# Kernel tuning notes

Hardware: AMD Instinct MI355X
Metric: run time of the kernel (lower is better)

## Reference

```python
import jax, jax.numpy as jnp
import numpy as np

N, D, E, L, H, F1, G, A = 4096, 256, 131072, 3, 4, 128, 16, 32

def setup_inputs() -> dict:
    key = jax.random.key(0)
    ks = jax.random.split(key, 12)
    s = lambda k, shape, fan: jax.random.normal(k, shape, jnp.float32) / np.sqrt(fan)
    return {
        "x": jax.random.normal(ks[0], (N, D), jnp.float32),
        "edge_attr": jax.random.uniform(ks[1], (E,), jnp.float32),
        "conv_Wself": s(ks[2], (L, D, D), D),
        "conv_Wnbr": s(ks[3], (L, D, D), D),
        "conv_b": jnp.zeros((L, D), jnp.float32),
        "bn_gamma": jnp.ones((L - 1, D), jnp.float32),
        "bn_beta": jnp.zeros((L - 1, D), jnp.float32),
        "bn_mean": jnp.zeros((L - 1, D), jnp.float32),
        "bn_var": jnp.ones((L - 1, D), jnp.float32),
        "Wqkv": s(ks[4], (3, D, D), D),
        "bqkv": jnp.zeros((3, D), jnp.float32),
        "Wo": s(ks[5], (D, D), D),
        "bo": jnp.zeros((D,), jnp.float32),
        "fc1_W": s(ks[6], (D, F1), D),
        "fc1_b": jnp.zeros((F1,), jnp.float32),
        "AW1": s(ks[7], (G, F1, A), F1),
        "Ab1": jnp.zeros((G, A), jnp.float32),
        "AW2": s(ks[8], (G, A, 1), A),
        "Ab2": jnp.zeros((G, 1), jnp.float32),
        "edge_index": jax.random.randint(ks[9], (2, E), 0, N, jnp.int32),
        "node_groups": jax.random.randint(ks[10], (N,), 0, G, jnp.int32),
    }


def reference(x, edge_attr, conv_Wself, conv_Wnbr, conv_b, bn_gamma, bn_beta,
              bn_mean, bn_var, Wqkv, bqkv, Wo, bo, fc1_W, fc1_b,
              AW1, Ab1, AW2, Ab2, edge_index, node_groups):
    src, dst = edge_index[0], edge_index[1]
    # message-passing conv stack (edge_attr only used by the last, non-attention layer)
    for i in range(L):
        msg = x[src]
        if i == L - 1:
            msg = msg * edge_attr[:, None]
        agg = jax.ops.segment_sum(msg, dst, num_segments=N)
        x = x @ conv_Wself[i] + agg @ conv_Wnbr[i] + conv_b[i]
        if i < L - 1:
            x = bn_gamma[i] * (x - bn_mean[i]) * jax.lax.rsqrt(bn_var[i] + 1e-5) + bn_beta[i]
            x = jax.nn.elu(x)
    # hierarchy self-attention over all N nodes (batch of 1), residual add
    dh = D // H
    q = (x @ Wqkv[0] + bqkv[0]).reshape(N, H, dh)
    k = (x @ Wqkv[1] + bqkv[1]).reshape(N, H, dh)
    v = (x @ Wqkv[2] + bqkv[2]).reshape(N, H, dh)
    scores = jnp.einsum('nhd,mhd->hnm', q, k) / np.sqrt(dh).astype(np.float32)
    attn = jax.nn.softmax(scores, axis=-1)
    o = jnp.einsum('hnm,mhd->nhd', attn, v).reshape(N, D) @ Wo + bo
    x = x + o
    feats = jax.nn.elu(x @ fc1_W + fc1_b)  # [N, F1]; dropout is eval no-op
    # MoE-style per-node group adapter routing: gather tiny MLP weights per node
    h = jax.nn.relu(jnp.einsum('nd,nda->na', feats, AW1[node_groups]) + Ab1[node_groups])
    out = jnp.einsum('na,nao->no', h, AW2[node_groups]) + Ab2[node_groups]  # [N, 1]
    return out
```

## Files before the change

### kernel.cpp

```cpp
#include <hip/hip_runtime.h>
#include <math.h>

#define NN   4096
#define DIM  256
#define NE   131072
#define NH   4
#define DH   64
#define F1D  128
#define NG   16
#define AD   32

typedef unsigned short u16;
typedef unsigned int   u32;
typedef _Float16 f16;
typedef __attribute__((ext_vector_type(8))) _Float16 half8;
typedef __attribute__((ext_vector_type(4))) float f32x4;

enum { EPI_BIAS = 0, EPI_BNELU = 1 };
enum { MEPI_WO = 0, MEPI_FC1 = 1 };

#define MFMA16(a, b, c) __builtin_amdgcn_mfma_f32_16x16x32_f16(a, b, c, 0, 0, 0)

__device__ inline u16 f2h(float x) { union { f16 f; u16 u; } c; c.f = (f16)x; return c.u; }
__device__ inline void split16(float x, u16& h, u16& l) {
    union { f16 f; u16 u; } ch, cl;
    ch.f = (f16)x;
    cl.f = (f16)(x - (float)ch.f);
    h = ch.u; l = cl.u;
}

__global__ void csr_count(const int* __restrict__ dst, int* __restrict__ cnt) {
    int e = blockIdx.x * 256 + threadIdx.x;
    atomicAdd(&cnt[dst[e]], 1);
}

__global__ __launch_bounds__(1024) void csr_scan(
    int* __restrict__ cnt, int* __restrict__ off)
{
    __shared__ int wsum[16];
    const int t = threadIdx.x;
    const int lane = t & 63;
    int4 v = *(const int4*)&cnt[t * 4];
    const int s = v.x + v.y + v.z + v.w;
    int acc = s;
    #pragma unroll
    for (int o = 1; o < 64; o <<= 1) {
        int u = __shfl_up(acc, o);
        if (lane >= o) acc += u;
    }
    if (lane == 63) wsum[t >> 6] = acc;
    __syncthreads();
    if (t < 16) {
        int w0 = wsum[t];
        int a2 = w0;
        #pragma unroll
        for (int o = 1; o < 16; o <<= 1) {
            int u = __shfl_up(a2, o);
            if (t >= o) a2 += u;
        }
        wsum[t] = a2 - w0;
    }
    __syncthreads();
    const int base = wsum[t >> 6] + (acc - s);
    off[t * 4 + 0] = base;
    off[t * 4 + 1] = base + v.x;
    off[t * 4 + 2] = base + v.x + v.y;
    off[t * 4 + 3] = base + v.x + v.y + v.z;
    *(int4*)&cnt[t * 4] = make_int4(0, 0, 0, 0);
    if (t == 1023) off[NN] = base + s;
}

__global__ void csr_fill(const int* __restrict__ dst, const int* __restrict__ src,
                         const float* __restrict__ eattr, const int* __restrict__ off,
                         int* __restrict__ cur, int* __restrict__ esrc,
                         float* __restrict__ ewt) {
    int e = blockIdx.x * 256 + threadIdx.x;
    int d = dst[e];
    int pos = off[d] + atomicAdd(&cur[d], 1);
    esrc[pos] = src[e];
    ewt[pos]  = eattr[e];
}

__global__ __launch_bounds__(256) void prep_kernel(
    const float* __restrict__ x,
    const float* __restrict__ Ws, const float* __restrict__ Wn,
    const float* __restrict__ Wqkv, const float* __restrict__ Wo,
    const float* __restrict__ fc1W,
    u16* __restrict__ xh, u16* __restrict__ xl,
    u16* __restrict__ wch, u16* __restrict__ wcl,
    u16* __restrict__ w4h, u16* __restrict__ w4l,
    u16* __restrict__ f1h, u16* __restrict__ f1l,
    int* __restrict__ cur)
{
    const int b = blockIdx.x;
    const int t = threadIdx.x;
    if (b < 1024) {
        const int gid = b * 256 + t;
        const float4 v = *(const float4*)&x[(size_t)gid * 4];
        u16 h[4], l[4];
        split16(v.x, h[0], l[0]); split16(v.y, h[1], l[1]);
        split16(v.z, h[2], l[2]); split16(v.w, h[3], l[3]);
        *(uint2*)&xh[(size_t)gid * 4] =
            make_uint2((u32)h[0] | ((u32)h[1] << 16), (u32)h[2] | ((u32)h[3] << 16));
        *(uint2*)&xl[(size_t)gid * 4] =
            make_uint2((u32)l[0] | ((u32)l[1] << 16), (u32)l[2] | ((u32)l[3] << 16));
    } else if (b < 1408) {
        const int gid = (b - 1024) * 256 + t;
        const int L = gid / 32768;
        const int rem = gid % 32768;
        const int m = rem / 128;
        const int k4 = (rem % 128) * 4;
        const float* S = Ws + (size_t)L * 65536;
        const float* Nb = Wn + (size_t)L * 65536;
        u16 h[4], l[4];
        #pragma unroll
        for (int j = 0; j < 4; ++j) {
            const int k = k4 + j;
            const float v = (k < 256) ? S[(size_t)k * 256 + m]
                                      : Nb[(size_t)(k - 256) * 256 + m];
            split16(v, h[j], l[j]);
        }
        const size_t o = (size_t)L * 131072 + (size_t)m * 512 + k4;
        *(uint2*)&wch[o] = make_uint2((u32)h[0] | ((u32)h[1] << 16), (u32)h[2] | ((u32)h[3] << 16));
        *(uint2*)&wcl[o] = make_uint2((u32)l[0] | ((u32)l[1] << 16), (u32)l[2] | ((u32)l[3] << 16));
    } else if (b < 1664) {
        const int gid = (b - 1408) * 256 + t;
        const int mat = gid / 16384;
        const int rem = gid % 16384;
        const int m = rem / 64;
        const int k4 = (rem % 64) * 4;
        const float* W = (mat < 3) ? Wqkv + (size_t)mat * 65536 : Wo;
        u16 h[4], l[4];
        #pragma unroll
        for (int j = 0; j < 4; ++j)
            split16(W[(size_t)(k4 + j) * 256 + m], h[j], l[j]);
        const size_t o = (size_t)mat * 65536 + (size_t)m * 256 + k4;
        *(uint2*)&w4h[o] = make_uint2((u32)h[0] | ((u32)h[1] << 16), (u32)h[2] | ((u32)h[3] << 16));
        *(uint2*)&w4l[o] = make_uint2((u32)l[0] | ((u32)l[1] << 16), (u32)l[2] | ((u32)l[3] << 16));
    } else if (b < 1696) {
        const int gid = (b - 1664) * 256 + t;
        const int m = gid / 64;
        const int k4 = (gid % 64) * 4;
        u16 h[4], l[4];
        #pragma unroll
        for (int j = 0; j < 4; ++j)
            split16(fc1W[(size_t)(k4 + j) * F1D + m], h[j], l[j]);
        const size_t o = (size_t)m * 256 + k4;
        *(uint2*)&f1h[o] = make_uint2((u32)h[0] | ((u32)h[1] << 16), (u32)h[2] | ((u32)h[3] << 16));
        *(uint2*)&f1l[o] = make_uint2((u32)l[0] | ((u32)l[1] << 16), (u32)l[2] | ((u32)l[3] << 16));
    } else {
        const int gid = (b - 1696) * 256 + t;
        if (gid < NN / 4) *(int4*)&cur[gid * 4] = make_int4(0, 0, 0, 0);
    }
}

template<bool LAST>
__global__ __launch_bounds__(256) void agg_kernel(
    const float* __restrict__ x, const int* __restrict__ esrc,
    const float* __restrict__ ewt, const int* __restrict__ off,
    u16* __restrict__ aggh, u16* __restrict__ aggl)
{
    const int node = blockIdx.x * 4 + (threadIdx.x >> 6);
    const int lane = threadIdx.x & 63;
    const int d4 = lane * 4;
    int j = off[node];
    const int j1 = off[node + 1];
    float4 acc = make_float4(0.f, 0.f, 0.f, 0.f);
    for (; j + 4 <= j1; j += 4) {
        const int s0 = esrc[j], s1 = esrc[j + 1], s2 = esrc[j + 2], s3 = esrc[j + 3];
        const float4 x0 = *(const float4*)&x[(size_t)s0 * DIM + d4];
        const float4 x1 = *(const float4*)&x[(size_t)s1 * DIM + d4];
        const float4 x2 = *(const float4*)&x[(size_t)s2 * DIM + d4];
        const float4 x3 = *(const float4*)&x[(size_t)s3 * DIM + d4];
        const float w0 = LAST ? ewt[j]     : 1.f;
        const float w1 = LAST ? ewt[j + 1] : 1.f;
        const float w2 = LAST ? ewt[j + 2] : 1.f;
        const float w3 = LAST ? ewt[j + 3] : 1.f;
        acc.x = fmaf(x0.x, w0, acc.x); acc.y = fmaf(x0.y, w0, acc.y);
        acc.z = fmaf(x0.z, w0, acc.z); acc.w = fmaf(x0.w, w0, acc.w);
        acc.x = fmaf(x1.x, w1, acc.x); acc.y = fmaf(x1.y, w1, acc.y);
        acc.z = fmaf(x1.z, w1, acc.z); acc.w = fmaf(x1.w, w1, acc.w);
        acc.x = fmaf(x2.x, w2, acc.x); acc.y = fmaf(x2.y, w2, acc.y);
        acc.z = fmaf(x2.z, w2, acc.z); acc.w = fmaf(x2.w, w2, acc.w);
        acc.x = fmaf(x3.x, w3, acc.x); acc.y = fmaf(x3.y, w3, acc.y);
        acc.z = fmaf(x3.z, w3, acc.z); acc.w = fmaf(x3.w, w3, acc.w);
    }
    for (; j < j1; ++j) {
        const int s = esrc[j];
        const float w = LAST ? ewt[j] : 1.f;
        const float4 xv = *(const float4*)&x[(size_t)s * DIM + d4];
        acc.x = fmaf(xv.x, w, acc.x); acc.y = fmaf(xv.y, w, acc.y);
        acc.z = fmaf(xv.z, w, acc.z); acc.w = fmaf(xv.w, w, acc.w);
    }
    u16 h[4], l[4];
    split16(acc.x, h[0], l[0]); split16(acc.y, h[1], l[1]);
    split16(acc.z, h[2], l[2]); split16(acc.w, h[3], l[3]);
    *(uint2*)&aggh[(size_t)node * DIM + d4] =
        make_uint2((u32)h[0] | ((u32)h[1] << 16), (u32)h[2] | ((u32)h[3] << 16));
    *(uint2*)&aggl[(size_t)node * DIM + d4] =
        make_uint2((u32)l[0] | ((u32)l[1] << 16), (u32)l[2] | ((u32)l[3] << 16));
}

template<int EPI>
__global__ __launch_bounds__(256) void conv_mfma(
    const u16* __restrict__ xh, const u16* __restrict__ xl,
    const u16* __restrict__ gh, const u16* __restrict__ gl,
    const u16* __restrict__ bth, const u16* __restrict__ btl,
    const float* __restrict__ bias,
    const float* __restrict__ gamma, const float* __restrict__ beta,
    const float* __restrict__ bnmean, const float* __restrict__ bnvar,
    float* __restrict__ outf, u16* __restrict__ oh, u16* __restrict__ ol)
{
    __shared__ u16 lds[4 * 4608];
    u16* As_h = lds;
    u16* As_l = lds + 4608;
    u16* Bs_h = lds + 9216;
    u16* Bs_l = lds + 13824;
    #define TKP 72

    const int tid  = threadIdx.x;
    const int row0 = blockIdx.y * 64;
    const int col0 = blockIdx.x * 64;

    const int w   = tid >> 6;
    const int l15 = tid & 15, h4 = (tid & 63) >> 4;
    const int rh  = w & 1, ch = w >> 1;
    const int lrow = tid & 63, lseg = tid >> 6;
    const int lc = lseg * 16;

    uint4 sah0, sah1, sal0, sal1, sbh0, sbh1, sbl0, sbl1;
    {
        const u16* pah = xh + (size_t)(row0 + lrow) * DIM + lc;
        const u16* pal = xl + (size_t)(row0 + lrow) * DIM + lc;
        const u16* pbh = bth + (size_t)(col0 + lrow) * 512 + lc;
        const u16* pbl = btl + (size_t)(col0 + lrow) * 512 + lc;
        sah0 = ((const uint4*)pah)[0]; sah1 = ((const uint4*)pah)[1];
        sal0 = ((const uint4*)pal)[0]; sal1 = ((const uint4*)pal)[1];
        sbh0 = ((const uint4*)pbh)[0]; sbh1 = ((const uint4*)pbh)[1];
        sbl0 = ((const uint4*)pbl)[0]; sbl1 = ((const uint4*)pbl)[1];
    }

    const f32x4 z4 = {0.f, 0.f, 0.f, 0.f};
    f32x4 acc[2][2] = {{z4, z4}, {z4, z4}};

    for (int kt = 0; kt < 8; ++kt) {
        *(uint4*)&As_h[lrow * TKP + lc]     = sah0;
        *(uint4*)&As_h[lrow * TKP + lc + 8] = sah1;
        *(uint4*)&As_l[lrow * TKP + lc]     = sal0;
        *(uint4*)&As_l[lrow * TKP + lc + 8] = sal1;
        *(uint4*)&Bs_h[lrow * TKP + lc]     = sbh0;
        *(uint4*)&Bs_h[lrow * TKP + lc + 8] = sbh1;
        *(uint4*)&Bs_l[lrow * TKP + lc]     = sbl0;
        *(uint4*)&Bs_l[lrow * TKP + lc + 8] = sbl1;
        if (kt + 1 < 8) {
            const int kn = kt + 1;
            const u16 *pah, *pal;
            if (kn < 4) {
                pah = xh + (size_t)(row0 + lrow) * DIM + kn * 64 + lc;
                pal = xl + (size_t)(row0 + lrow) * DIM + kn * 64 + lc;
            } else {
                pah = gh + (size_t)(row0 + lrow) * DIM + (kn - 4) * 64 + lc;
                pal = gl + (size_t)(row0 + lrow) * DIM + (kn - 4) * 64 + lc;
            }
            const u16* pbh = bth + (size_t)(col0 + lrow) * 512 + kn * 64 + lc;
            const u16* pbl = btl + (size_t)(col0 + lrow) * 512 + kn * 64 + lc;
            sah0 = ((const uint4*)pah)[0]; sah1 = ((const uint4*)pah)[1];
            sal0 = ((const uint4*)pal)[0]; sal1 = ((const uint4*)pal)[1];
            sbh0 = ((const uint4*)pbh)[0]; sbh1 = ((const uint4*)pbh)[1];
            sbl0 = ((const uint4*)pbl)[0]; sbl1 = ((const uint4*)pbl)[1];
        }
        __syncthreads();

        __builtin_amdgcn_s_setprio(1);
        #pragma unroll
        for (int kc = 0; kc < 2; ++kc) {
            const int dc = kc * 32 + h4 * 8;
            half8 afh[2], afl[2], bfh[2], bfl[2];
            #pragma unroll
            for (int ab = 0; ab < 2; ++ab) {
                const int r = rh * 32 + ab * 16 + l15;
                afh[ab] = *(const half8*)&As_h[r * TKP + dc];
                afl[ab] = *(const half8*)&As_l[r * TKP + dc];
            }
            #pragma unroll
            for (int bb = 0; bb < 2; ++bb) {
                const int r = ch * 32 + bb * 16 + l15;
                bfh[bb] = *(const half8*)&Bs_h[r * TKP + dc];
                bfl[bb] = *(const half8*)&Bs_l[r * TKP + dc];
            }
            #pragma unroll
            for (int ab = 0; ab < 2; ++ab)
                #pragma unroll
                for (int bb = 0; bb < 2; ++bb) {
                    acc[ab][bb] = MFMA16(afh[ab], bfh[bb], acc[ab][bb]);
                    acc[ab][bb] = MFMA16(afh[ab], bfl[bb], acc[ab][bb]);
                    acc[ab][bb] = MFMA16(afl[ab], bfh[bb], acc[ab][bb]);
                }
        }
        __builtin_amdgcn_s_setprio(0);
        __syncthreads();
    }

    #pragma unroll
    for (int ab = 0; ab < 2; ++ab)
        #pragma unroll
        for (int bb = 0; bb < 2; ++bb) {
            const int c  = col0 + ch * 32 + bb * 16 + l15;
            const int r0 = row0 + rh * 32 + ab * 16 + h4 * 4;
            #pragma unroll
            for (int i = 0; i < 4; ++i) {
                const int r = r0 + i;
                float t = acc[ab][bb][i] + bias[c];
                if (EPI == EPI_BNELU) {
                    t = gamma[c] * (t - bnmean[c]) * rsqrtf(bnvar[c] + 1e-5f) + beta[c];
                    t = t > 0.f ? t : expm1f(t);
                }
                outf[(size_t)r * DIM + c] = t;
                u16 hh, ll;
                split16(t, hh, ll);
                oh[(size_t)r * DIM + c] = hh;
                ol[(size_t)r * DIM + c] = ll;
            }
        }
    #undef TKP
}

__global__ __launch_bounds__(256) void qkv_mfma(
    const u16* __restrict__ xh, const u16* __restrict__ xl,
    const u16* __restrict__ wth, const u16* __restrict__ wtl,
    const float* __restrict__ bias,
    u16* __restrict__ qh_o, u16* __restrict__ ql_o,
    u16* __restrict__ kh_o, u16* __restrict__ kl_o,
    u16* __restrict__ vt_o)
{
    __shared__ u16 lds[4 * 4608];
    u16* As_h = lds;
    u16* As_l = lds + 4608;
    u16* Bs_h = lds + 9216;
    u16* Bs_l = lds + 13824;
    #define TKP 72

    const int tid  = threadIdx.x;
    const int row0 = blockIdx.y * 64;
    const int mat  = blockIdx.x >> 2;
    const int col0 = (blockIdx.x & 3) * 64;
    const float* biasp = bias + mat * DIM;

    const int w   = tid >> 6;
    const int l15 = tid & 15, h4 = (tid & 63) >> 4;
    const int rh  = w & 1, ch = w >> 1;
    const int lrow = tid & 63, lseg = tid >> 6;
    const int lc = lseg * 16;

    const size_t brow = (size_t)(mat * 256 + col0 + lrow) * 256;
    uint4 sah0, sah1, sal0, sal1, sbh0, sbh1, sbl0, sbl1;
    {
        const u16* pah = xh + (size_t)(row0 + lrow) * DIM + lc;
        const u16* pal = xl + (size_t)(row0 + lrow) * DIM + lc;
        sah0 = ((const uint4*)pah)[0]; sah1 = ((const uint4*)pah)[1];
        sal0 = ((const uint4*)pal)[0]; sal1 = ((const uint4*)pal)[1];
        sbh0 = ((const uint4*)(wth + brow + lc))[0]; sbh1 = ((const uint4*)(wth + brow + lc))[1];
        sbl0 = ((const uint4*)(wtl + brow + lc))[0]; sbl1 = ((const uint4*)(wtl + brow + lc))[1];
    }

    const f32x4 z4 = {0.f, 0.f, 0.f, 0.f};
    f32x4 acc[2][2] = {{z4, z4}, {z4, z4}};

    for (int kt = 0; kt < 4; ++kt) {
        *(uint4*)&As_h[lrow * TKP + lc]     = sah0;
        *(uint4*)&As_h[lrow * TKP + lc + 8] = sah1;
        *(uint4*)&As_l[lrow * TKP + lc]     = sal0;
        *(uint4*)&As_l[lrow * TKP + lc + 8] = sal1;
        *(uint4*)&Bs_h[lrow * TKP + lc]     = sbh0;
        *(uint4*)&Bs_h[lrow * TKP + lc + 8] = sbh1;
        *(uint4*)&Bs_l[lrow * TKP + lc]     = sbl0;
        *(uint4*)&Bs_l[lrow * TKP + lc + 8] = sbl1;
        if (kt + 1 < 4) {
            const int kb = (kt + 1) * 64 + lc;
            const u16* pah = xh + (size_t)(row0 + lrow) * DIM + kb;
            const u16* pal = xl + (size_t)(row0 + lrow) * DIM + kb;
            sah0 = ((const uint4*)pah)[0]; sah1 = ((const uint4*)pah)[1];
            sal0 = ((const uint4*)pal)[0]; sal1 = ((const uint4*)pal)[1];
            sbh0 = ((const uint4*)(wth + brow + kb))[0]; sbh1 = ((const uint4*)(wth + brow + kb))[1];
            sbl0 = ((const uint4*)(wtl + brow + kb))[0]; sbl1 = ((const uint4*)(wtl + brow + kb))[1];
        }
        __syncthreads();

        __builtin_amdgcn_s_setprio(1);
        #pragma unroll
        for (int kc = 0; kc < 2; ++kc) {
            const int dc = kc * 32 + h4 * 8;
            half8 afh[2], afl[2], bfh[2], bfl[2];
            #pragma unroll
            for (int ab = 0; ab < 2; ++ab) {
                const int r = rh * 32 + ab * 16 + l15;
                afh[ab] = *(const half8*)&As_h[r * TKP + dc];
                afl[ab] = *(const half8*)&As_l[r * TKP + dc];
            }
            #pragma unroll
            for (int bb = 0; bb < 2; ++bb) {
                const int r = ch * 32 + bb * 16 + l15;
                bfh[bb] = *(const half8*)&Bs_h[r * TKP + dc];
                bfl[bb] = *(const half8*)&Bs_l[r * TKP + dc];
            }
            #pragma unroll
            for (int ab = 0; ab < 2; ++ab)
                #pragma unroll
                for (int bb = 0; bb < 2; ++bb) {
                    acc[ab][bb] = MFMA16(afh[ab], bfh[bb], acc[ab][bb]);
                    acc[ab][bb] = MFMA16(afh[ab], bfl[bb], acc[ab][bb]);
                    acc[ab][bb] = MFMA16(afl[ab], bfh[bb], acc[ab][bb]);
                }
        }
        __builtin_amdgcn_s_setprio(0);
        __syncthreads();
    }

    const float s = (mat == 0) ? 0.125f : 1.0f;
    u16* oph = (mat == 0) ? qh_o : kh_o;
    u16* opl = (mat == 0) ? ql_o : kl_o;
    #pragma unroll
    for (int ab = 0; ab < 2; ++ab)
        #pragma unroll
        for (int bb = 0; bb < 2; ++bb) {
            const int c  = col0 + ch * 32 + bb * 16 + l15;
            const int r0 = row0 + rh * 32 + ab * 16 + h4 * 4;
            if (mat < 2) {
                #pragma unroll
                for (int i = 0; i < 4; ++i) {
                    const int r = r0 + i;
                    const float t = (acc[ab][bb][i] + biasp[c]) * s;
                    u16 hh, ll;
                    split16(t, hh, ll);
                    oph[(size_t)r * DIM + c] = hh;
                    opl[(size_t)r * DIM + c] = ll;
                }
            } else {
                u16 v[4];
                #pragma unroll
                for (int i = 0; i < 4; ++i)
                    v[i] = f2h(acc[ab][bb][i] + biasp[c]);
                *(uint2*)&vt_o[(size_t)c * NN + r0] =
                    make_uint2((u32)v[0] | ((u32)v[1] << 16), (u32)v[2] | ((u32)v[3] << 16));
            }
        }
    #undef TKP
}

template<int MEPI>
__global__ __launch_bounds__(256) void mfma_gemm(
    const u16* __restrict__ Ah, const u16* __restrict__ Al,
    const u16* __restrict__ Bth, const u16* __restrict__ Btl,
    const float* __restrict__ bias, const float* __restrict__ resid,
    float* __restrict__ outf, u16* __restrict__ outh, u16* __restrict__ outl,
    int K, int M)
{
    __shared__ u16 lds[4 * 4608];
    u16* As_h = lds;
    u16* As_l = lds + 4608;
    u16* Bs_h = lds + 9216;
    u16* Bs_l = lds + 13824;
    #define TKP 72

    const int tid  = threadIdx.x;
    const int row0 = blockIdx.y * 64;
    const int col0 = blockIdx.x * 64;

    const int w   = tid >> 6;
    const int l15 = tid & 15, h4 = (tid & 63) >> 4;
    const int rh  = w & 1, ch = w >> 1;
    const int lrow = tid & 63, lseg = tid >> 6;
    const int lc = lseg * 16;

    uint4 sah0, sah1, sal0, sal1, sbh0, sbh1, sbl0, sbl1;
    {
        const u16* pa0 = Ah  + (size_t)(row0 + lrow) * K + lc;
        const u16* pa1 = Al  + (size_t)(row0 + lrow) * K + lc;
        const u16* pb0 = Bth + (size_t)(col0 + lrow) * K + lc;
        const u16* pb1 = Btl + (size_t)(col0 + lrow) * K + lc;
        sah0 = ((const uint4*)pa0)[0]; sah1 = ((const uint4*)pa0)[1];
        sal0 = ((const uint4*)pa1)[0]; sal1 = ((const uint4*)pa1)[1];
        sbh0 = ((const uint4*)pb0)[0]; sbh1 = ((const uint4*)pb0)[1];
        sbl0 = ((const uint4*)pb1)[0]; sbl1 = ((const uint4*)pb1)[1];
    }

    const f32x4 z4 = {0.f, 0.f, 0.f, 0.f};
    f32x4 acc[2][2] = {{z4, z4}, {z4, z4}};
    const int NKT2 = K / 64;

    for (int kt = 0; kt < NKT2; ++kt) {
        *(uint4*)&As_h[lrow * TKP + lc]     = sah0;
        *(uint4*)&As_h[lrow * TKP + lc + 8] = sah1;
        *(uint4*)&As_l[lrow * TKP + lc]     = sal0;
        *(uint4*)&As_l[lrow * TKP + lc + 8] = sal1;
        *(uint4*)&Bs_h[lrow * TKP + lc]     = sbh0;
        *(uint4*)&Bs_h[lrow * TKP + lc + 8] = sbh1;
        *(uint4*)&Bs_l[lrow * TKP + lc]     = sbl0;
        *(uint4*)&Bs_l[lrow * TKP + lc + 8] = sbl1;
        if (kt + 1 < NKT2) {
            const int kb = (kt + 1) * 64 + lc;
            const u16* pa0 = Ah  + (size_t)(row0 + lrow) * K + kb;
            const u16* pa1 = Al  + (size_t)(row0 + lrow) * K + kb;
            const u16* pb0 = Bth + (size_t)(col0 + lrow) * K + kb;
            const u16* pb1 = Btl + (size_t)(col0 + lrow) * K + kb;
            sah0 = ((const uint4*)pa0)[0]; sah1 = ((const uint4*)pa0)[1];
            sal0 = ((const uint4*)pa1)[0]; sal1 = ((const uint4*)pa1)[1];
            sbh0 = ((const uint4*)pb0)[0]; sbh1 = ((const uint4*)pb0)[1];
            sbl0 = ((const uint4*)pb1)[0]; sbl1 = ((const uint4*)pb1)[1];
        }
        __syncthreads();

        __builtin_amdgcn_s_setprio(1);
        #pragma unroll
        for (int kc = 0; kc < 2; ++kc) {
            const int dc = kc * 32 + h4 * 8;
            half8 afh[2], afl[2], bfh[2], bfl[2];
            #pragma unroll
            for (int ab = 0; ab < 2; ++ab) {
                const int r = rh * 32 + ab * 16 + l15;
                afh[ab] = *(const half8*)&As_h[r * TKP + dc];
                afl[ab] = *(const half8*)&As_l[r * TKP + dc];
            }
            #pragma unroll
            for (int bb = 0; bb < 2; ++bb) {
                const int r = ch * 32 + bb * 16 + l15;
                bfh[bb] = *(const half8*)&Bs_h[r * TKP + dc];
                bfl[bb] = *(const half8*)&Bs_l[r * TKP + dc];
            }
            #pragma unroll
            for (int ab = 0; ab < 2; ++ab)
                #pragma unroll
                for (int bb = 0; bb < 2; ++bb) {
                    acc[ab][bb] = MFMA16(afh[ab], bfh[bb], acc[ab][bb]);
                    acc[ab][bb] = MFMA16(afh[ab], bfl[bb], acc[ab][bb]);
                    acc[ab][bb] = MFMA16(afl[ab], bfh[bb], acc[ab][bb]);
                }
        }
        __builtin_amdgcn_s_setprio(0);
        __syncthreads();
    }

    #pragma unroll
    for (int ab = 0; ab < 2; ++ab)
        #pragma unroll
        for (int bb = 0; bb < 2; ++bb) {
            const int c  = col0 + ch * 32 + bb * 16 + l15;
            const int r0 = row0 + rh * 32 + ab * 16 + h4 * 4;
            #pragma unroll
            for (int i = 0; i < 4; ++i) {
                const int r = r0 + i;
                float t = acc[ab][bb][i] + bias[c];
                if (MEPI == MEPI_WO) {
                    t += resid[(size_t)r * M + c];
                    u16 hh, ll;
                    split16(t, hh, ll);
                    outh[(size_t)r * M + c] = hh;
                    outl[(size_t)r * M + c] = ll;
                } else {
                    t = t > 0.f ? t : expm1f(t);
                    outf[(size_t)r * M + c] = t;
                }
            }
        }
    #undef TKP
}

#define QB 64
#define KB 64
#define NSPLIT 4
#define NKT (NN / KB)
#define KP 72

__global__ __launch_bounds__(256, 3) void attn_kernel(
    const u16* __restrict__ qhi, const u16* __restrict__ qlo,
    const u16* __restrict__ khi, const u16* __restrict__ klo,
    const u16* __restrict__ vT,
    float* __restrict__ op0, float* __restrict__ op1,
    float* __restrict__ op2, float* __restrict__ op3,
    float* __restrict__ mpart, float* __restrict__ lpart)
{
    __shared__ u16 lds[18560];
    u16* Kh = lds;
    u16* Kl = lds + 4608;
    u16* Vt = lds + 9216;
    u16* Pb = lds + 13824;
    u16* Qh = lds;
    u16* Ql = lds + 4608;
    float* frow = (float*)(lds + 18432);

    const int tid = threadIdx.x;
    const int h   = blockIdx.y;
    const int q0  = blockIdx.x * QB;
    const int sp  = blockIdx.z;
    const int kt0 = sp * (NKT / NSPLIT);
    const int kt1 = kt0 + NKT / NSPLIT;

    const int w   = tid >> 6;
    const int l   = tid & 63;
    const int l15 = l & 15, h4 = l >> 4;

    const int lrow = tid & 63, lseg = tid >> 6;
    const int gq = h * DH + lseg * 16;

    {
        const u16* s0 = qhi + (size_t)(q0 + lrow) * DIM + gq;
        const u16* s1 = qlo + (size_t)(q0 + lrow) * DIM + gq;
        uint4 a = ((const uint4*)s0)[0], b = ((const uint4*)s0)[1];
        uint4 c = ((const uint4*)s1)[0], d = ((const uint4*)s1)[1];
        *(uint4*)&Qh[lrow * KP + lseg * 16]     = a;
        *(uint4*)&Qh[lrow * KP + lseg * 16 + 8] = b;
        *(uint4*)&Ql[lrow * KP + lseg * 16]     = c;
        *(uint4*)&Ql[lrow * KP + lseg * 16 + 8] = d;
    }

    auto load_tile = [&](int kt_ld, uint4& k0, uint4& k1, uint4& l0, uint4& l1,
                         uint4& v0, uint4& v1) {
        const int key0 = kt_ld * KB;
        const u16* s0 = khi + (size_t)(key0 + lrow) * DIM + gq;
        const u16* s1 = klo + (size_t)(key0 + lrow) * DIM + gq;
        const u16* s2 = vT + (size_t)(h * DH + lrow) * NN + key0 + lseg * 16;
        k0 = ((const uint4*)s0)[0]; k1 = ((const uint4*)s0)[1];
        l0 = ((const uint4*)s1)[0]; l1 = ((const uint4*)s1)[1];
        v0 = ((const uint4*)s2)[0]; v1 = ((const uint4*)s2)[1];
    };

    uint4 kA0, kA1, lA0, lA1, vA0, vA1;
    uint4 kB0, kB1, lB0, lB1, vB0, vB1;
    load_tile(kt0,     kA0, kA1, lA0, lA1, vA0, vA1);
    load_tile(kt0 + 1, kB0, kB1, lB0, lB1, vB0, vB1);
    __syncthreads();

    half8 qf[2][2];
    #pragma unroll
    for (int kc = 0; kc < 2; ++kc) {
        const int r = w * 16 + l15;
        const int dc = kc * 32 + h4 * 8;
        qf[kc][0] = *(const half8*)&Qh[r * KP + dc];
        qf[kc][1] = *(const half8*)&Ql[r * KP + dc];
    }
    __syncthreads();

    const f32x4 z4 = {0.f, 0.f, 0.f, 0.f};
    f32x4 oacc[4] = {z4, z4, z4, z4};
    float m_run[4], l_run[4];
    #pragma unroll
    for (int i = 0; i < 4; ++i) { m_run[i] = -3.0e38f; l_run[i] = 0.f; }

    auto tile_body = [&](uint4& k0, uint4& k1, uint4& l0, uint4& l1,
                         uint4& v0, uint4& v1, int ldnext) {
        *(uint4*)&Kh[lrow * KP + lseg * 16]     = k0;
        *(uint4*)&Kh[lrow * KP + lseg * 16 + 8] = k1;
        *(uint4*)&Kl[lrow * KP + lseg * 16]     = l0;
        *(uint4*)&Kl[lrow * KP + lseg * 16 + 8] = l1;
        *(uint4*)&Vt[lrow * KP + lseg * 16]     = v0;
        *(uint4*)&Vt[lrow * KP + lseg * 16 + 8] = v1;
        if (ldnext < kt1)
            load_tile(ldnext, k0, k1, l0, l1, v0, v1);
        __syncthreads();

        f32x4 sc[4] = {z4, z4, z4, z4};
        __builtin_amdgcn_s_setprio(1);
        #pragma unroll
        for (int kc = 0; kc < 2; ++kc) {
            const int dc = kc * 32 + h4 * 8;
            half8 kfh[4], kfl[4];
            #pragma unroll
            for (int kcb = 0; kcb < 4; ++kcb) {
                const int r = kcb * 16 + l15;
                kfh[kcb] = *(const half8*)&Kh[r * KP + dc];
                kfl[kcb] = *(const half8*)&Kl[r * KP + dc];
            }
            #pragma unroll
            for (int kcb = 0; kcb < 4; ++kcb) {
                sc[kcb] = MFMA16(qf[kc][0], kfh[kcb], sc[kcb]);
                sc[kcb] = MFMA16(qf[kc][0], kfl[kcb], sc[kcb]);
                sc[kcb] = MFMA16(qf[kc][1], kfh[kcb], sc[kcb]);
            }
        }
        __builtin_amdgcn_s_setprio(0);
        float p[4][4], fr[4];
        #pragma unroll
        for (int i = 0; i < 4; ++i) {
            float pm = fmaxf(fmaxf(sc[0][i], sc[1][i]), fmaxf(sc[2][i], sc[3][i]));
            #pragma unroll
            for (int off = 1; off < 16; off <<= 1)
                pm = fmaxf(pm, __shfl_xor(pm, off));
            const float mnew = fmaxf(m_run[i], pm);
            fr[i] = __expf(m_run[i] - mnew);
            m_run[i] = mnew;
            p[0][i] = __expf(sc[0][i] - mnew);
            p[1][i] = __expf(sc[1][i] - mnew);
            p[2][i] = __expf(sc[2][i] - mnew);
            p[3][i] = __expf(sc[3][i] - mnew);
            float ls = (p[0][i] + p[1][i]) + (p[2][i] + p[3][i]);
            #pragma unroll
            for (int off = 1; off < 16; off <<= 1) ls += __shfl_xor(ls, off);
            l_run[i] = l_run[i] * fr[i] + ls;
        }
        #pragma unroll
        for (int kcb = 0; kcb < 4; ++kcb) {
            const int kk = kcb * 16 + l15;
            #pragma unroll
            for (int i = 0; i < 4; ++i)
                Pb[(w * 16 + h4 * 4 + i) * KP + kk] = f2h(p[kcb][i]);
        }
        if (l15 == 0) {
            #pragma unroll
            for (int i = 0; i < 4; ++i)
                frow[w * 16 + h4 * 4 + i] = fr[i];
        }
        const float frq = frow[w * 16 + l15];
        #pragma unroll
        for (int db = 0; db < 4; ++db) oacc[db] *= frq;
        __builtin_amdgcn_s_setprio(1);
        #pragma unroll
        for (int kc = 0; kc < 2; ++kc) {
            const half8 pf = *(const half8*)&Pb[(w * 16 + l15) * KP + kc * 32 + h4 * 8];
            #pragma unroll
            for (int db = 0; db < 4; ++db) {
                const half8 vf = *(const half8*)&Vt[(db * 16 + l15) * KP + kc * 32 + h4 * 8];
                oacc[db] = MFMA16(vf, pf, oacc[db]);
            }
        }
        __builtin_amdgcn_s_setprio(0);
        __syncthreads();
    };

    for (int kt = kt0; kt < kt1; kt += 2) {
        tile_body(kA0, kA1, lA0, lA1, vA0, vA1, kt + 2);
        tile_body(kB0, kB1, lB0, lB1, vB0, vB1, kt + 3);
    }

    float* ob = (sp == 0) ? op0 : ((sp == 1) ? op1 : ((sp == 2) ? op2 : op3));
    #pragma unroll
    for (int db = 0; db < 4; ++db)
        *(f32x4*)&ob[(size_t)(q0 + w * 16 + l15) * DIM + h * DH + db * 16 + h4 * 4] = oacc[db];
    if (l15 == 0) {
        #pragma unroll
        for (int i = 0; i < 4; ++i) {
            const int r = w * 16 + h4 * 4 + i;
            mpart[((size_t)sp * NN + q0 + r) * NH + h] = m_run[i];
            lpart[((size_t)sp * NN + q0 + r) * NH + h] = l_run[i];
        }
    }
}

__global__ __launch_bounds__(256) void attn_combine(
    const float* __restrict__ o0, const float* __restrict__ o1,
    const float* __restrict__ o2, const float* __restrict__ o3,
    const float* __restrict__ mp, const float* __restrict__ lp,
    u16* __restrict__ ohi, u16* __restrict__ olo)
{
    const int gid = blockIdx.x * 256 + threadIdx.x;
    const int row = gid >> 6;
    const int c4  = (gid & 63) * 4;
    const int h   = c4 >> 6;
    float m[4], wgt[4];
    #pragma unroll
    for (int z = 0; z < 4; ++z) m[z] = mp[((size_t)z * NN + row) * NH + h];
    const float M = fmaxf(fmaxf(m[0], m[1]), fmaxf(m[2], m[3]));
    float den = 0.f;
    #pragma unroll
    for (int z = 0; z < 4; ++z) {
        wgt[z] = __expf(m[z] - M);
        den += lp[((size_t)z * NN + row) * NH + h] * wgt[z];
    }
    const float inv = 1.f / den;
    const float4 a = *(const float4*)&o0[(size_t)row * DIM + c4];
    const float4 b = *(const float4*)&o1[(size_t)row * DIM + c4];
    const float4 c = *(const float4*)&o2[(size_t)row * DIM + c4];
    const float4 d = *(const float4*)&o3[(size_t)row * DIM + c4];
    float r[4];
    r[0] = (a.x * wgt[0] + b.x * wgt[1] + c.x * wgt[2] + d.x * wgt[3]) * inv;
    r[1] = (a.y * wgt[0] + b.y * wgt[1] + c.y * wgt[2] + d.y * wgt[3]) * inv;
    r[2] = (a.z * wgt[0] + b.z * wgt[1] + c.z * wgt[2] + d.z * wgt[3]) * inv;
    r[3] = (a.w * wgt[0] + b.w * wgt[1] + c.w * wgt[2] + d.w * wgt[3]) * inv;
    u16 hh[4], ll[4];
    #pragma unroll
    for (int j = 0; j < 4; ++j) split16(r[j], hh[j], ll[j]);
    *(uint2*)&ohi[(size_t)row * DIM + c4] =
        make_uint2((u32)hh[0] | ((u32)hh[1] << 16), (u32)hh[2] | ((u32)hh[3] << 16));
    *(uint2*)&olo[(size_t)row * DIM + c4] =
        make_uint2((u32)ll[0] | ((u32)ll[1] << 16), (u32)ll[2] | ((u32)ll[3] << 16));
}

__global__ __launch_bounds__(64) void adapter_kernel(
    const float* __restrict__ feats, const int* __restrict__ grp,
    const float* __restrict__ AW1, const float* __restrict__ Ab1,
    const float* __restrict__ AW2, const float* __restrict__ Ab2,
    float* __restrict__ out)
{
    const int n = blockIdx.x;
    const int lane = threadIdx.x;
    __shared__ float f[F1D];
    f[lane]      = feats[(size_t)n * F1D + lane];
    f[lane + 64] = feats[(size_t)n * F1D + 64 + lane];
    __syncthreads();
    const int g = grp[n];
    const float* W1 = AW1 + (size_t)g * F1D * AD;
    const int a = lane & 31;
    const int half = lane >> 5;
    float hsum = 0.f;
    for (int d = 0; d < 64; ++d)
        hsum = fmaf(f[half * 64 + d], W1[(half * 64 + d) * AD + a], hsum);
    hsum += __shfl_xor(hsum, 32);
    hsum = fmaxf(hsum + Ab1[g * AD + a], 0.f);
    float p = hsum * AW2[g * AD + a];
    #pragma unroll
    for (int mm = 1; mm < 32; mm <<= 1) p += __shfl_xor(p, mm);
    if (lane == 0) out[n] = p + Ab2[g];
}

extern "C" void kernel_launch(void* const* d_in, const int* in_sizes, int n_in,
                              void* d_out, int out_size, void* d_ws, size_t ws_size,
                              hipStream_t stream)
{
    const float* x_in   = (const float*)d_in[0];
    const float* eattr  = (const float*)d_in[1];
    const float* Wself  = (const float*)d_in[2];
    const float* Wnbr   = (const float*)d_in[3];
    const float* convb  = (const float*)d_in[4];
    const float* gamma  = (const float*)d_in[5];
    const float* beta   = (const float*)d_in[6];
    const float* bnmean = (const float*)d_in[7];
    const float* bnvar  = (const float*)d_in[8];
    const float* Wqkv   = (const float*)d_in[9];
    const float* bqkv   = (const float*)d_in[10];
    const float* Wo     = (const float*)d_in[11];
    const float* bo     = (const float*)d_in[12];
    const float* fc1W   = (const float*)d_in[13];
    const float* fc1b   = (const float*)d_in[14];
    const float* AW1    = (const float*)d_in[15];
    const float* Ab1    = (const float*)d_in[16];
    const float* AW2    = (const float*)d_in[17];
    const float* Ab2    = (const float*)d_in[18];
    const int*   eidx   = (const int*)d_in[19];
    const int*   grp    = (const int*)d_in[20];
    const int* srcArr = eidx;
    const int* dstArr = eidx + NE;

    float* fws = (float*)d_ws;
    const size_t NM = (size_t)NN * DIM;
    float* bufA  = fws;
    float* bufB  = fws + NM;
    float* bufC  = fws + 2 * NM;
    float* feats = fws + 3 * NM;
    float* mpart = fws + 3 * NM + NM / 2;
    float* lpart = mpart + 4 * NN * NH;
    u16* up = (u16*)(lpart + 4 * NN * NH);
    u16* xpAh = up;             u16* xpAl = xpAh + NM;
    u16* xpBh = xpAl + NM;      u16* xpBl = xpBh + NM;
    u16* aggh = xpBl + NM;      u16* aggl = aggh + NM;
    u16* qh = aggl + NM;        u16* ql = qh + NM;
    u16* kh = ql + NM;          u16* kl = kh + NM;
    u16* vt = kl + NM;
    u16* wcath = vt + NM;
    u16* wcatl = wcath + 3 * 131072;
    u16* wt4h  = wcatl + 3 * 131072;
    u16* wt4l  = wt4h + 4 * 65536;
    u16* fc1h  = wt4l + 4 * 65536;
    u16* fc1l  = fc1h + 32768;
    int*   esrc = (int*)(fc1l + 32768);
    float* ewt  = (float*)(esrc + NE);
    int* off    = (int*)(ewt + NE);
    int* cur    = off + NN + 1;
    float* outp = (float*)d_out;

    float* op2 = (float*)xpAh;
    float* op3 = (float*)xpBh;

    prep_kernel<<<1700, 256, 0, stream>>>(
        x_in, Wself, Wnbr, Wqkv, Wo, fc1W,
        xpAh, xpAl, wcath, wcatl, wt4h, wt4l, fc1h, fc1l, cur);

    csr_count<<<NE / 256, 256, 0, stream>>>(dstArr, cur);
    csr_scan<<<1, 1024, 0, stream>>>(cur, off);
    csr_fill<<<NE / 256, 256, 0, stream>>>(dstArr, srcArr, eattr, off, cur, esrc, ewt);

    const dim3 gc(DIM / 64, NN / 64);
    const int rgrid = NN * DIM / 4 / 256;

    agg_kernel<false><<<NN / 4, 256, 0, stream>>>(x_in, esrc, ewt, off, aggh, aggl);
    conv_mfma<EPI_BNELU><<<gc, 256, 0, stream>>>(
        xpAh, xpAl, aggh, aggl, wcath, wcatl, convb,
        gamma, beta, bnmean, bnvar, bufA, xpBh, xpBl);
    agg_kernel<false><<<NN / 4, 256, 0, stream>>>(bufA, esrc, ewt, off, aggh, aggl);
    conv_mfma<EPI_BNELU><<<gc, 256, 0, stream>>>(
        xpBh, xpBl, aggh, aggl, wcath + 131072, wcatl + 131072, convb + DIM,
        gamma + DIM, beta + DIM, bnmean + DIM, bnvar + DIM, bufC, xpAh, xpAl);
    agg_kernel<true><<<NN / 4, 256, 0, stream>>>(bufC, esrc, ewt, off, aggh, aggl);
    conv_mfma<EPI_BIAS><<<gc, 256, 0, stream>>>(
        xpAh, xpAl, aggh, aggl, wcath + 262144, wcatl + 262144, convb + 2 * DIM,
        nullptr, nullptr, nullptr, nullptr, bufA, xpBh, xpBl);

    qkv_mfma<<<dim3(12, NN / 64), 256, 0, stream>>>(
        xpBh, xpBl, wt4h, wt4l, bqkv, qh, ql, kh, kl, vt);

    attn_kernel<<<dim3(NN / QB, NH, NSPLIT), 256, 0, stream>>>(
        qh, ql, kh, kl, vt, bufB, bufC, op2, op3, mpart, lpart);
    attn_combine<<<rgrid, 256, 0, stream>>>(
        bufB, bufC, op2, op3, mpart, lpart, qh, ql);

    mfma_gemm<MEPI_WO><<<gc, 256, 0, stream>>>(
        qh, ql, wt4h + 3 * 65536, wt4l + 3 * 65536, bo, bufA,
        nullptr, kh, kl, DIM, DIM);

    mfma_gemm<MEPI_FC1><<<dim3(F1D / 64, NN / 64), 256, 0, stream>>>(
        kh, kl, fc1h, fc1l, fc1b, nullptr, feats, nullptr, nullptr, DIM, F1D);

    adapter_kernel<<<NN, 64, 0, stream>>>(feats, grp, AW1, Ab1, AW2, Ab2, outp);
}
```

Before: 244.5 us.

## Double-buffer K/V tiles in attention LDS and halve conv GEMM row tile

The attention kernel now keeps two LDS buffers for the K/V tiles. It stages the next tile into the alternate buffer while computing on the current one, which drops the register-held second tile and the barrier between staging and compute. Occupancy is lowered to 2 blocks per SM to make room for the larger LDS. Separately, the conv GEMM row tile shrinks from 64 to 32 rows, doubling the grid to improve CU utilisation on this small problem, at the cost of more B-tile reloads.

```diff
diff --git a/kernel.cpp b/kernel.cpp
--- a/kernel.cpp
+++ b/kernel.cpp
@@ -211,61 +211,58 @@
     const float* __restrict__ bnmean, const float* __restrict__ bnvar,
     float* __restrict__ outf, u16* __restrict__ oh, u16* __restrict__ ol)
 {
-    __shared__ u16 lds[4 * 4608];
+    __shared__ u16 lds[13824];
     u16* As_h = lds;
-    u16* As_l = lds + 4608;
-    u16* Bs_h = lds + 9216;
-    u16* Bs_l = lds + 13824;
+    u16* As_l = lds + 2304;
+    u16* Bs_h = lds + 4608;
+    u16* Bs_l = lds + 9216;
     #define TKP 72
 
     const int tid  = threadIdx.x;
-    const int row0 = blockIdx.y * 64;
+    const int row0 = blockIdx.y * 32;
     const int col0 = blockIdx.x * 64;
 
     const int w   = tid >> 6;
     const int l15 = tid & 15, h4 = (tid & 63) >> 4;
     const int rh  = w & 1, ch = w >> 1;
-    const int lrow = tid & 63, lseg = tid >> 6;
-    const int lc = lseg * 16;
-
-    uint4 sah0, sah1, sal0, sal1, sbh0, sbh1, sbl0, sbl1;
+    const int arow = tid >> 3, acs = (tid & 7) * 8;
+    const int brow = tid & 63, bseg = tid >> 6;
+    const int bc = bseg * 16;
+
+    uint4 sah, sal, sbh0, sbh1, sbl0, sbl1;
     {
-        const u16* pah = xh + (size_t)(row0 + lrow) * DIM + lc;
-        const u16* pal = xl + (size_t)(row0 + lrow) * DIM + lc;
-        const u16* pbh = bth + (size_t)(col0 + lrow) * 512 + lc;
-        const u16* pbl = btl + (size_t)(col0 + lrow) * 512 + lc;
-        sah0 = ((const uint4*)pah)[0]; sah1 = ((const uint4*)pah)[1];
-        sal0 = ((const uint4*)pal)[0]; sal1 = ((const uint4*)pal)[1];
+        sah = *((const uint4*)&xh[(size_t)(row0 + arow) * DIM + acs]);
+        sal = *((const uint4*)&xl[(size_t)(row0 + arow) * DIM + acs]);
+        const u16* pbh = bth + (size_t)(col0 + brow) * 512 + bc;
+        const u16* pbl = btl + (size_t)(col0 + brow) * 512 + bc;
         sbh0 = ((const uint4*)pbh)[0]; sbh1 = ((const uint4*)pbh)[1];
         sbl0 = ((const uint4*)pbl)[0]; sbl1 = ((const uint4*)pbl)[1];
     }
 
     const f32x4 z4 = {0.f, 0.f, 0.f, 0.f};
-    f32x4 acc[2][2] = {{z4, z4}, {z4, z4}};
+    f32x4 acc[2] = {z4, z4};
 
     for (int kt = 0; kt < 8; ++kt) {
-        *(uint4*)&As_h[lrow * TKP + lc]     = sah0;
-        *(uint4*)&As_h[lrow * TKP + lc + 8] = sah1;
-        *(uint4*)&As_l[lrow * TKP + lc]     = sal0;
-        *(uint4*)&As_l[lrow * TKP + lc + 8] = sal1;
-        *(uint4*)&Bs_h[lrow * TKP + lc]     = sbh0;
-        *(uint4*)&Bs_h[lrow * TKP + lc + 8] = sbh1;
-        *(uint4*)&Bs_l[lrow * TKP + lc]     = sbl0;
-        *(uint4*)&Bs_l[lrow * TKP + lc + 8] = sbl1;
+        *(uint4*)&As_h[arow * TKP + acs] = sah;
+        *(uint4*)&As_l[arow * TKP + acs] = sal;
+        *(uint4*)&Bs_h[brow * TKP + bc]     = sbh0;
+        *(uint4*)&Bs_h[brow * TKP + bc + 8] = sbh1;
+        *(uint4*)&Bs_l[brow * TKP + bc]     = sbl0;
+        *(uint4*)&Bs_l[brow * TKP + bc + 8] = sbl1;
         if (kt + 1 < 8) {
             const int kn = kt + 1;
             const u16 *pah, *pal;
             if (kn < 4) {
-                pah = xh + (size_t)(row0 + lrow) * DIM + kn * 64 + lc;
-                pal = xl + (size_t)(row0 + lrow) * DIM + kn * 64 + lc;
+                pah = xh + (size_t)(row0 + arow) * DIM + kn * 64 + acs;
+                pal = xl + (size_t)(row0 + arow) * DIM + kn * 64 + acs;
             } else {
-                pah = gh + (size_t)(row0 + lrow) * DIM + (kn - 4) * 64 + lc;
-                pal = gl + (size_t)(row0 + lrow) * DIM + (kn - 4) * 64 + lc;
-            }
-            const u16* pbh = bth + (size_t)(col0 + lrow) * 512 + kn * 64 + lc;
-            const u16* pbl = btl + (size_t)(col0 + lrow) * 512 + kn * 64 + lc;
-            sah0 = ((const uint4*)pah)[0]; sah1 = ((const uint4*)pah)[1];
-            sal0 = ((const uint4*)pal)[0]; sal1 = ((const uint4*)pal)[1];
+                pah = gh + (size_t)(row0 + arow) * DIM + (kn - 4) * 64 + acs;
+                pal = gl + (size_t)(row0 + arow) * DIM + (kn - 4) * 64 + acs;
+            }
+            sah = *((const uint4*)pah);
+            sal = *((const uint4*)pal);
+            const u16* pbh = bth + (size_t)(col0 + brow) * 512 + kn * 64 + bc;
+            const u16* pbl = btl + (size_t)(col0 + brow) * 512 + kn * 64 + bc;
             sbh0 = ((const uint4*)pbh)[0]; sbh1 = ((const uint4*)pbh)[1];
             sbl0 = ((const uint4*)pbl)[0]; sbl1 = ((const uint4*)pbl)[1];
         }
@@ -275,13 +272,9 @@
         #pragma unroll
         for (int kc = 0; kc < 2; ++kc) {
             const int dc = kc * 32 + h4 * 8;
-            half8 afh[2], afl[2], bfh[2], bfl[2];
-            #pragma unroll
-            for (int ab = 0; ab < 2; ++ab) {
-                const int r = rh * 32 + ab * 16 + l15;
-                afh[ab] = *(const half8*)&As_h[r * TKP + dc];
-                afl[ab] = *(const half8*)&As_l[r * TKP + dc];
-            }
+            half8 afh, afl, bfh[2], bfl[2];
+            afh = *(const half8*)&As_h[(rh * 16 + l15) * TKP + dc];
+            afl = *(const half8*)&As_l[(rh * 16 + l15) * TKP + dc];
             #pragma unroll
             for (int bb = 0; bb < 2; ++bb) {
                 const int r = ch * 32 + bb * 16 + l15;
@@ -289,39 +282,35 @@
                 bfl[bb] = *(const half8*)&Bs_l[r * TKP + dc];
             }
             #pragma unroll
-            for (int ab = 0; ab < 2; ++ab)
-                #pragma unroll
-                for (int bb = 0; bb < 2; ++bb) {
-                    acc[ab][bb] = MFMA16(afh[ab], bfh[bb], acc[ab][bb]);
-                    acc[ab][bb] = MFMA16(afh[ab], bfl[bb], acc[ab][bb]);
-                    acc[ab][bb] = MFMA16(afl[ab], bfh[bb], acc[ab][bb]);
-                }
+            for (int bb = 0; bb < 2; ++bb) {
+                acc[bb] = MFMA16(afh, bfh[bb], acc[bb]);
+                acc[bb] = MFMA16(afh, bfl[bb], acc[bb]);
+                acc[bb] = MFMA16(afl, bfh[bb], acc[bb]);
+            }
         }
         __builtin_amdgcn_s_setprio(0);
         __syncthreads();
     }
 
     #pragma unroll
-    for (int ab = 0; ab < 2; ++ab)
-        #pragma unroll
-        for (int bb = 0; bb < 2; ++bb) {
-            const int c  = col0 + ch * 32 + bb * 16 + l15;
-            const int r0 = row0 + rh * 32 + ab * 16 + h4 * 4;
-            #pragma unroll
-            for (int i = 0; i < 4; ++i) {
-                const int r = r0 + i;
-                float t = acc[ab][bb][i] + bias[c];
-                if (EPI == EPI_BNELU) {
-                    t = gamma[c] * (t - bnmean[c]) * rsqrtf(bnvar[c] + 1e-5f) + beta[c];
-                    t = t > 0.f ? t : expm1f(t);
-                }
-                outf[(size_t)r * DIM + c] = t;
-                u16 hh, ll;
-                split16(t, hh, ll);
-                oh[(size_t)r * DIM + c] = hh;
-                ol[(size_t)r * DIM + c] = ll;
-            }
-        }
+    for (int bb = 0; bb < 2; ++bb) {
+        const int c  = col0 + ch * 32 + bb * 16 + l15;
+        const int r0 = row0 + rh * 16 + h4 * 4;
+        #pragma unroll
+        for (int i = 0; i < 4; ++i) {
+            const int r = r0 + i;
+            float t = acc[bb][i] + bias[c];
+            if (EPI == EPI_BNELU) {
+                t = gamma[c] * (t - bnmean[c]) * rsqrtf(bnvar[c] + 1e-5f) + beta[c];
+                t = t > 0.f ? t : expm1f(t);
+            }
+            outf[(size_t)r * DIM + c] = t;
+            u16 hh, ll;
+            split16(t, hh, ll);
+            oh[(size_t)r * DIM + c] = hh;
+            ol[(size_t)r * DIM + c] = ll;
+        }
+    }
     #undef TKP
 }
 
@@ -571,7 +560,7 @@
 #define NKT (NN / KB)
 #define KP 72
 
-__global__ __launch_bounds__(256, 3) void attn_kernel(
+__global__ __launch_bounds__(256, 2) void attn_kernel(
     const u16* __restrict__ qhi, const u16* __restrict__ qlo,
     const u16* __restrict__ khi, const u16* __restrict__ klo,
     const u16* __restrict__ vT,
@@ -579,14 +568,17 @@
     float* __restrict__ op2, float* __restrict__ op3,
     float* __restrict__ mpart, float* __restrict__ lpart)
 {
-    __shared__ u16 lds[18560];
-    u16* Kh = lds;
-    u16* Kl = lds + 4608;
-    u16* Vt = lds + 9216;
-    u16* Pb = lds + 13824;
-    u16* Qh = lds;
-    u16* Ql = lds + 4608;
-    float* frow = (float*)(lds + 18432);
+    __shared__ u16 lds[32384];
+    u16* Kh0 = lds;
+    u16* Kl0 = lds + 4608;
+    u16* Vt0 = lds + 9216;
+    u16* Kh1 = lds + 13824;
+    u16* Kl1 = lds + 18432;
+    u16* Vt1 = lds + 23040;
+    u16* Pb  = lds + 27648;
+    u16* Qh  = lds;
+    u16* Ql  = lds + 4608;
+    float* frow = (float*)(lds + 32256);
 
     const int tid = threadIdx.x;
     const int h   = blockIdx.y;
@@ -596,9 +588,7 @@
     const int kt1 = kt0 + NKT / NSPLIT;
 
     const int w   = tid >> 6;
-    const int l   = tid & 63;
-    const int l15 = l & 15, h4 = l >> 4;
-
+    const int l15 = tid & 15, h4 = (tid & 63) >> 4;
     const int lrow = tid & 63, lseg = tid >> 6;
     const int gq = h * DH + lseg * 16;
 
@@ -613,21 +603,17 @@
         *(uint4*)&Ql[lrow * KP + lseg * 16 + 8] = d;
     }
 
-    auto load_tile = [&](int kt_ld, uint4& k0, uint4& k1, uint4& l0, uint4& l1,
-                         uint4& v0, uint4& v1) {
+    uint4 rk0, rk1, rl0, rl1, rv0, rv1;
+    auto load_tile = [&](int kt_ld) {
         const int key0 = kt_ld * KB;
         const u16* s0 = khi + (size_t)(key0 + lrow) * DIM + gq;
         const u16* s1 = klo + (size_t)(key0 + lrow) * DIM + gq;
         const u16* s2 = vT + (size_t)(h * DH + lrow) * NN + key0 + lseg * 16;
-        k0 = ((const uint4*)s0)[0]; k1 = ((const uint4*)s0)[1];
-        l0 = ((const uint4*)s1)[0]; l1 = ((const uint4*)s1)[1];
-        v0 = ((const uint4*)s2)[0]; v1 = ((const uint4*)s2)[1];
+        rk0 = ((const uint4*)s0)[0]; rk1 = ((const uint4*)s0)[1];
+        rl0 = ((const uint4*)s1)[0]; rl1 = ((const uint4*)s1)[1];
+        rv0 = ((const uint4*)s2)[0]; rv1 = ((const uint4*)s2)[1];
     };
-
-    uint4 kA0, kA1, lA0, lA1, vA0, vA1;
-    uint4 kB0, kB1, lB0, lB1, vB0, vB1;
-    load_tile(kt0,     kA0, kA1, lA0, lA1, vA0, vA1);
-    load_tile(kt0 + 1, kB0, kB1, lB0, lB1, vB0, vB1);
+    load_tile(kt0);
     __syncthreads();
 
     half8 qf[2][2];
@@ -640,23 +626,29 @@
     }
     __syncthreads();
 
+    auto stage_to = [&](u16* Kh, u16* Kl, u16* Vt) {
+        *(uint4*)&Kh[lrow * KP + lseg * 16]     = rk0;
+        *(uint4*)&Kh[lrow * KP + lseg * 16 + 8] = rk1;
+        *(uint4*)&Kl[lrow * KP + lseg * 16]     = rl0;
+        *(uint4*)&Kl[lrow * KP + lseg * 16 + 8] = rl1;
+        *(uint4*)&Vt[lrow * KP + lseg * 16]     = rv0;
+        *(uint4*)&Vt[lrow * KP + lseg * 16 + 8] = rv1;
+    };
+
+    stage_to(Kh0, Kl0, Vt0);
+    load_tile(kt0 + 1);
+    __syncthreads();
+
     const f32x4 z4 = {0.f, 0.f, 0.f, 0.f};
     f32x4 oacc[4] = {z4, z4, z4, z4};
     float m_run[4], l_run[4];
     #pragma unroll
     for (int i = 0; i < 4; ++i) { m_run[i] = -3.0e38f; l_run[i] = 0.f; }
 
-    auto tile_body = [&](uint4& k0, uint4& k1, uint4& l0, uint4& l1,
-                         uint4& v0, uint4& v1, int ldnext) {
-        *(uint4*)&Kh[lrow * KP + lseg * 16]     = k0;
-        *(uint4*)&Kh[lrow * KP + lseg * 16 + 8] = k1;
-        *(uint4*)&Kl[lrow * KP + lseg * 16]     = l0;
-        *(uint4*)&Kl[lrow * KP + lseg * 16 + 8] = l1;
-        *(uint4*)&Vt[lrow * KP + lseg * 16]     = v0;
-        *(uint4*)&Vt[lrow * KP + lseg * 16 + 8] = v1;
-        if (ldnext < kt1)
-            load_tile(ldnext, k0, k1, l0, l1, v0, v1);
-        __syncthreads();
+    auto tile_body = [&](int t, u16* Kc, u16* Lc, u16* Vc,
+                         u16* Kn, u16* Ln, u16* Vn) {
+        if (t + 1 < kt1) stage_to(Kn, Ln, Vn);
+        if (t + 2 < kt1) load_tile(t + 2);
 
         f32x4 sc[4] = {z4, z4, z4, z4};
         __builtin_amdgcn_s_setprio(1);
@@ -667,8 +659,8 @@
             #pragma unroll
             for (int kcb = 0; kcb < 4; ++kcb) {
                 const int r = kcb * 16 + l15;
-                kfh[kcb] = *(const half8*)&Kh[r * KP + dc];
-                kfl[kcb] = *(const half8*)&Kl[r * KP + dc];
+                kfh[kcb] = *(const half8*)&Kc[r * KP + dc];
+                kfl[kcb] = *(const half8*)&Lc[r * KP + dc];
             }
             #pragma unroll
             for (int kcb = 0; kcb < 4; ++kcb) {
@@ -718,7 +710,7 @@
             const half8 pf = *(const half8*)&Pb[(w * 16 + l15) * KP + kc * 32 + h4 * 8];
             #pragma unroll
             for (int db = 0; db < 4; ++db) {
-                const half8 vf = *(const half8*)&Vt[(db * 16 + l15) * KP + kc * 32 + h4 * 8];
+                const half8 vf = *(const half8*)&Vc[(db * 16 + l15) * KP + kc * 32 + h4 * 8];
                 oacc[db] = MFMA16(vf, pf, oacc[db]);
             }
         }
@@ -726,9 +718,9 @@
         __syncthreads();
     };
 
-    for (int kt = kt0; kt < kt1; kt += 2) {
-        tile_body(kA0, kA1, lA0, lA1, vA0, vA1, kt + 2);
-        tile_body(kB0, kB1, lB0, lB1, vB0, vB1, kt + 3);
+    for (int t = kt0; t < kt1; t += 2) {
+        tile_body(t,     Kh0, Kl0, Vt0, Kh1, Kl1, Vt1);
+        tile_body(t + 1, Kh1, Kl1, Vt1, Kh0, Kl0, Vt0);
     }
 
     float* ob = (sp == 0) ? op0 : ((sp == 1) ? op1 : ((sp == 2) ? op2 : op3));
@@ -877,7 +869,7 @@
     csr_scan<<<1, 1024, 0, stream>>>(cur, off);
     csr_fill<<<NE / 256, 256, 0, stream>>>(dstArr, srcArr, eattr, off, cur, esrc, ewt);
 
-    const dim3 gc(DIM / 64, NN / 64);
+    const dim3 gc(DIM / 64, NN / 32);
     const int rgrid = NN * DIM / 4 / 256;
 
     agg_kernel<false><<<NN / 4, 256, 0, stream>>>(x_in, esrc, ewt, off, aggh, aggl);
@@ -901,7 +893,7 @@
     attn_combine<<<rgrid, 256, 0, stream>>>(
         bufB, bufC, op2, op3, mpart, lpart, qh, ql);
 
-    mfma_gemm<MEPI_WO><<<gc, 256, 0, stream>>>(
+    mfma_gemm<MEPI_WO><<<dim3(DIM / 64, NN / 64), 256, 0, stream>>>(
         qh, ql, wt4h + 3 * 65536, wt4l + 3 * 65536, bo, bufA,
         nullptr, kh, kl, DIM, DIM);
 
```

New measurement: 243.1 us. Within noise of the previous version (-0.6%).
